# Performance work log

Measured on AMD Instinct MI355X. Metric: run time of the kernel, lower is better.

Reference implementation:

```python
import jax, jax.numpy as jnp
import numpy as np

HEADS = 4
KSIZE = 3
EPS = 1e-5


def conv2d(x, w, b, stride=1, padding=0, dilation=1):
    out = jax.lax.conv_general_dilated(
        x, w, (stride, stride), [(padding, padding)] * 2,
        rhs_dilation=(dilation, dilation),
        dimension_numbers=('NCHW', 'OIHW', 'NCHW'))
    return out + b[None, :, None, None]


def conv1x1(x, w, b):
    # w: (O, I, 1, 1)
    return jnp.einsum('oi,bihw->bohw', w[:, :, 0, 0], x) + b[None, :, None, None]


def batchnorm(x, gamma, beta, mean, var):
    inv = jax.lax.rsqrt(var + EPS)
    return (x - mean[None, :, None, None]) * (inv * gamma)[None, :, None, None] + beta[None, :, None, None]


def lrelu(x):
    return jax.nn.leaky_relu(x, 0.05)


def sasa(kv1, qmap, kv2, Wq, bq, Wkv, bkv):
    b, c, h, w = qmap.shape
    d = Wq.shape[0] // HEADS
    scale = d ** -0.5
    q = conv1x1(qmap, Wq, bq)                                   # b (n d) h w
    q = q.reshape(b, HEADS, d, h * w).transpose(0, 1, 3, 2) * scale  # b n x d

    def branch(kvmap):
        # pad BEFORE 1x1 conv (padded pixels attend with value = bias), matching torch
        p = jnp.pad(kvmap, ((0, 0), (0, 0), (1, 1), (1, 1)))
        kvp = conv1x1(p, Wkv, bkv)                              # b (n d) h+2 w+2
        # sliding 3x3 windows (k=v in the original: to_kv applied twice to same input)
        wins = jnp.stack([kvp[:, :, i:i + h, j:j + w]
                          for i in range(KSIZE) for j in range(KSIZE)], axis=2)  # b nd 9 h w
        kv = wins.reshape(b, HEADS, d, KSIZE * KSIZE, h * w).transpose(0, 1, 4, 3, 2)  # b n x y d
        logits = jnp.einsum('bnxd,bnxyd->bnxy', q, kv)
        wgt = jax.nn.softmax(logits, axis=-1)
        return jnp.einsum('bnxy,bnxyd->bnxd', wgt, kv)

    out = (branch(kv1) + branch(kv2)) * 0.5                     # b n x d
    return out.transpose(0, 1, 3, 2).reshape(b, HEADS * d, h, w)


def setup_inputs() -> dict:
    key = jax.random.key(0)
    ks = jax.random.split(key, 12)
    B, Cin, Cout, H, W = 2, 64, 128, 128, 128
    f32 = jnp.float32
    inp = {
        'x0': jax.random.normal(ks[0], (B, Cin, H, W), f32),
        'x1': jax.random.normal(ks[1], (B, Cin, H, W), f32),
        'x2': jax.random.normal(ks[2], (B, Cin, H, W), f32),
        # BN params (eval mode, reps=2)
        'gamma0': jnp.ones((Cin,), f32), 'beta0': jnp.zeros((Cin,), f32),
        'mean0': jnp.zeros((Cin,), f32), 'var0': jnp.ones((Cin,), f32),
        'gamma1': jnp.ones((Cout,), f32), 'beta1': jnp.zeros((Cout,), f32),
        'mean1': jnp.zeros((Cout,), f32), 'var1': jnp.ones((Cout,), f32),
        # channel-adjust 1x1 conv (residual path, i==0)
        'W_adj': jax.random.normal(ks[3], (Cout, Cin, 1, 1), f32) * 0.05,
        'b_adj': jnp.zeros((Cout,), f32),
        # 3x3 dilated convs
        'W_conv0': jax.random.normal(ks[4], (Cout, Cin, 3, 3), f32) * 0.05,
        'b_conv0': jnp.zeros((Cout,), f32),
        'W_conv1': jax.random.normal(ks[5], (Cout, Cout, 3, 3), f32) * 0.05,
        'b_conv1': jnp.zeros((Cout,), f32),
        # SASA projections
        'Wq': jax.random.normal(ks[6], (Cout, Cout, 1, 1), f32) * 0.05,
        'bq': jnp.zeros((Cout,), f32),
        'Wkv': jax.random.normal(ks[7], (Cout, Cout, 1, 1), f32) * 0.05,
        'bkv': jnp.zeros((Cout,), f32),
        # conv pooling (3x3 stride 2 pad 1)
        'W_pool': jax.random.normal(ks[8], (Cout, Cout, 3, 3), f32) * 0.05,
        'b_pool': jnp.zeros((Cout,), f32),
    }
    return inp


def reference(x0, x1, x2,
              gamma0, beta0, mean0, var0, gamma1, beta1, mean1, var1,
              W_adj, b_adj, W_conv0, b_conv0, W_conv1, b_conv1,
              Wq, bq, Wkv, bkv, W_pool, b_pool):
    dil = 1

    def rep(x, i):
        if i == 0:
            x = batchnorm(x, gamma0, beta0, mean0, var0)
            res = conv1x1(x, W_adj, b_adj)
            x = conv2d(x, W_conv0, b_conv0, 1, dil, dil)
        else:
            x = batchnorm(x, gamma1, beta1, mean1, var1)
            res = x
            x = conv2d(x, W_conv1, b_conv1, 1, dil, dil)
        return lrelu(x + res)

    n0, n1, n2 = x0, x1, x2
    for i in range(2):
        n0 = rep(n0, i)
        n1 = rep(n1, i)
        n2 = rep(n2, i)

    n1 = sasa(n0, n1, n2, Wq, bq, Wkv, bkv)
    pass_layer = n1
    n0 = conv2d(n0, W_pool, b_pool, stride=2, padding=1)
    n1 = conv2d(n1, W_pool, b_pool, stride=2, padding=1)
    n2 = conv2d(n2, W_pool, b_pool, stride=2, padding=1)
    return (n0, n1, n2, pass_layer)
```

## Files before the change

### kernel.cpp

```cpp
#include <hip/hip_runtime.h>
#include <cstdint>
#include <cstddef>

typedef __bf16 bf16x8 __attribute__((ext_vector_type(8)));
typedef float f32x4 __attribute__((ext_vector_type(4)));
typedef unsigned short u16x8 __attribute__((ext_vector_type(8)));
typedef unsigned int u32x4 __attribute__((ext_vector_type(4)));

#define AS1 __attribute__((address_space(1)))
#define AS3 __attribute__((address_space(3)))

__device__ __forceinline__ void gload16(const void* g, void* l) {
    __builtin_amdgcn_global_load_lds((AS1 unsigned int*)(unsigned long long)g,
                                     (AS3 unsigned int*)l, 16, 0, 0);
}

__device__ __forceinline__ unsigned short f2b(float f) {
    unsigned u = __builtin_bit_cast(unsigned, f);
    return (unsigned short)((u + 0x7fffu + ((u >> 16) & 1u)) >> 16);
}
__device__ __forceinline__ float b2f(unsigned short h) {
    return __builtin_bit_cast(float, ((unsigned)h) << 16);
}

static constexpr int HW = 16384;

__global__ __launch_bounds__(256) void zero_borders_kernel(
    unsigned short* X0, unsigned short* X1, unsigned short* X2,
    unsigned short* F0, unsigned short* F1, unsigned short* F2,
    unsigned short* G0, unsigned short* G1, unsigned short* G2)
{
    int z = blockIdx.z;
    unsigned short* p; int C;
    switch (z) {
        case 0: p = X0; C = 64; break;
        case 1: p = X1; C = 64; break;
        case 2: p = X2; C = 64; break;
        case 3: p = F0; C = 128; break;
        case 4: p = F1; C = 128; break;
        case 5: p = F2; C = 128; break;
        case 6: p = G0; C = 128; break;
        case 7: p = G1; C = 128; break;
        default: p = G2; C = 128; break;
    }
    int chunks = C >> 3;
    int total = 2 * 516 * chunks;
    int idx = blockIdx.x * 256 + threadIdx.x;
    if (idx >= total) return;
    int cb = idx % chunks;
    int pidx = idx / chunks;
    int n = pidx / 516;
    int b = pidx % 516;
    int y, x;
    if (b < 130)      { y = 0;       x = b; }
    else if (b < 260) { y = 129;     x = b - 130; }
    else if (b < 388) { y = b - 259; x = 0; }
    else              { y = b - 387; x = 129; }
    u32x4 zz = {0u, 0u, 0u, 0u};
    *(u32x4*)(p + ((size_t)((n * 130 + y) * 130 + x)) * C + cb * 8) = zz;
}

__global__ __launch_bounds__(256) void zero_one_kernel(unsigned short* p)
{
    int idx = blockIdx.x * 256 + threadIdx.x;
    if (idx >= 2 * 516 * 16) return;
    int cb = idx & 15;
    int pidx = idx >> 4;
    int n = pidx / 516;
    int b = pidx % 516;
    int y, x;
    if (b < 130)      { y = 0;       x = b; }
    else if (b < 260) { y = 129;     x = b - 130; }
    else if (b < 388) { y = b - 259; x = 0; }
    else              { y = b - 387; x = 129; }
    u32x4 zz = {0u, 0u, 0u, 0u};
    *(u32x4*)(p + ((size_t)((n * 130 + y) * 130 + x)) * 128 + cb * 8) = zz;
}

__global__ __launch_bounds__(256) void pack_kernel(
    const float* Wc0, const float* Wadj, const float* Wc1,
    const float* Wq, const float* Wkv, const float* Wpool,
    const float* bc0, const float* badj,
    const float* g1, const float* be1, const float* m1, const float* v1,
    unsigned short* W0p, unsigned short* W1p, unsigned short* Wqp,
    unsigned short* Wkvp, unsigned short* Wpp,
    float* b0sum, float* s1a, float* t1a)
{
    int z = blockIdx.z;
    int idx = blockIdx.x * 256 + threadIdx.x;
    if (z == 5) {
        if (idx < 128) {
            int co = idx;
            b0sum[co] = bc0[co] + badj[co];
            float s = g1[co] * rsqrtf(v1[co] + 1e-5f);
            s1a[co] = s;
            t1a[co] = be1[co] - m1[co] * s;
        }
        return;
    }
    int CIN, NTAP; unsigned short* dst;
    switch (z) {
        case 0: CIN = 64;  NTAP = 10; dst = W0p;  break;
        case 1: CIN = 128; NTAP = 10; dst = W1p;  break;
        case 2: CIN = 128; NTAP = 1;  dst = Wqp;  break;
        case 3: CIN = 128; NTAP = 1;  dst = Wkvp; break;
        default: CIN = 128; NTAP = 9; dst = Wpp;  break;
    }
    int KCN = CIN / 32;
    int count = NTAP * KCN * 512;
    if (idx >= count) return;
    int lane = idx & 63;
    int m = (idx >> 6) & 7;
    int rest = idx >> 9;
    int kc = rest % KCN;
    int tap = rest / KCN;
    int co = m * 16 + (lane & 15);
    int cib = kc * 32 + ((lane >> 4) << 3);
    unsigned short vals[8];
#pragma unroll
    for (int j = 0; j < 8; ++j) {
        int ci = cib + j;
        float v;
        if (z == 0)       v = (tap < 9) ? Wc0[((size_t)co * 64 + ci) * 9 + tap] : Wadj[co * 64 + ci];
        else if (z == 1)  v = (tap < 9) ? Wc1[((size_t)co * 128 + ci) * 9 + tap] : (co == ci ? 1.0f : 0.0f);
        else if (z == 2)  v = Wq[co * 128 + ci];
        else if (z == 3)  v = Wkv[co * 128 + ci];
        else              v = Wpool[((size_t)co * 128 + ci) * 9 + tap];
        vals[j] = f2b(v);
    }
    u32x4 pk;
    pk.x = vals[0] | ((unsigned)vals[1] << 16);
    pk.y = vals[2] | ((unsigned)vals[3] << 16);
    pk.z = vals[4] | ((unsigned)vals[5] << 16);
    pk.w = vals[6] | ((unsigned)vals[7] << 16);
    *(u32x4*)(dst + (size_t)idx * 8) = pk;
}

__global__ __launch_bounds__(256) void prep_kernel(
    const float* x0, const float* x1, const float* x2,
    const float* g0, const float* be0, const float* me0, const float* va0,
    unsigned short* X0, unsigned short* X1, unsigned short* X2)
{
    const int y = blockIdx.x;
    const int mz = blockIdx.y;
    const int map = mz >> 1, n = mz & 1;
    const float* in = (map == 0 ? x0 : map == 1 ? x1 : x2) + (size_t)n * 64 * HW + y * 128;
    unsigned short* out = (map == 0 ? X0 : map == 1 ? X1 : X2)
                          + ((size_t)(n * 130 + y + 1) * 130 + 1) * 64;
    const int x = threadIdx.x & 127;
    for (int cb = threadIdx.x >> 7; cb < 8; cb += 2) {
        unsigned short vals[8];
#pragma unroll
        for (int j = 0; j < 8; ++j) {
            int ci = cb * 8 + j;
            float s = g0[ci] * rsqrtf(va0[ci] + 1e-5f);
            float t = be0[ci] - me0[ci] * s;
            vals[j] = f2b(in[(size_t)ci * HW + x] * s + t);
        }
        u32x4 pk;
        pk.x = vals[0] | ((unsigned)vals[1] << 16);
        pk.y = vals[2] | ((unsigned)vals[3] << 16);
        pk.z = vals[4] | ((unsigned)vals[5] << 16);
        pk.w = vals[6] | ((unsigned)vals[7] << 16);
        *(u32x4*)(out + (size_t)x * 64 + cb * 8) = pk;
    }
}

template <int CIN, int EPI>
__global__ __launch_bounds__(256, 6) void conv3_kernel(
    const unsigned short* I0, const unsigned short* I1, const unsigned short* I2,
    const unsigned short* Wp, const float* bA, const float* bB, const float* bC,
    unsigned short* O0, unsigned short* O1, unsigned short* O2)
{
    constexpr int KCN = CIN / 32;
    constexpr int TKY[10] = {0,0,0,1,1,1,2,2,2,1};
    constexpr int TKX[10] = {0,1,2,0,1,2,0,1,2,1};
    const int tid = threadIdx.x;
    const int lane = tid & 63;
    const int l15 = lane & 15, l4 = lane >> 4;
    const int wv = tid >> 6;
    const int pxh = wv & 1;
    const int coq = wv >> 1;
    const int bid = blockIdx.x;
    const int wid = (bid & 7) * 192 + (bid >> 3);
    const int ch = wid & 1;
    const int y  = (wid >> 1) & 127;
    const int mz = wid >> 8;
    const int map = mz >> 1, n = mz & 1;
    const unsigned short* In = (map == 0 ? I0 : map == 1 ? I1 : I2) + (size_t)n * 130 * 130 * CIN;
    unsigned short* On = (map == 0 ? O0 : map == 1 ? O1 : O2) + (size_t)n * 130 * 130 * 128;

    __shared__ __align__(16) unsigned short stage[3 * 130 * 4 * 8];

    f32x4 acc[2][4];
#pragma unroll
    for (int a = 0; a < 2; ++a)
#pragma unroll
        for (int b = 0; b < 4; ++b) acc[a][b] = (f32x4){0.f, 0.f, 0.f, 0.f};

    const int px0 = pxh * 64;
    const u32x4* Ap = (const u32x4*)Wp;

    for (int kc = 0; kc < KCN; ++kc) {
        if (kc) __syncthreads();
        for (int idx = tid; idx < 1560; idx += 256) {
            int r = idx / 520;
            int rem = idx - r * 520;
            int xx = rem >> 2;
            int slot = rem & 3;
            int cd = slot ^ ((xx >> 1) & 3);
            const unsigned short* src = In + ((size_t)(y + r) * 130 + xx) * CIN + kc * 32 + cd * 8;
            gload16(src, stage + (size_t)(idx & ~63) * 8);
        }
        __syncthreads();
#pragma unroll
        for (int t = 0; t < 10; ++t) {
            const int ky = TKY[t], kx = TKX[t];
            u32x4 a[2];
#pragma unroll
            for (int mi = 0; mi < 2; ++mi)
                a[mi] = Ap[((size_t)(t * KCN + kc) * 8 + ch * 4 + coq * 2 + mi) * 64 + lane];
            bf16x8 bv[4];
#pragma unroll
            for (int nf = 0; nf < 4; ++nf) {
                int xx = px0 + nf * 16 + l15 + kx;
                int slot = l4 ^ ((xx >> 1) & 3);
                bv[nf] = *(const bf16x8*)(stage + ((size_t)(ky * 130 + xx) * 4 + slot) * 8);
            }
#pragma unroll
            for (int mi = 0; mi < 2; ++mi) {
                bf16x8 av = __builtin_bit_cast(bf16x8, a[mi]);
#pragma unroll
                for (int nf = 0; nf < 4; ++nf)
                    acc[mi][nf] = __builtin_amdgcn_mfma_f32_16x16x32_bf16(av, bv[nf], acc[mi][nf], 0, 0, 0);
            }
        }
    }
#pragma unroll
    for (int mi = 0; mi < 2; ++mi) {
#pragma unroll
        for (int nf = 0; nf < 4; ++nf) {
            int px = px0 + nf * 16 + l15;
            int cobase = (ch * 4 + coq * 2 + mi) * 16 + l4 * 4;
            float t4[4];
#pragma unroll
            for (int r = 0; r < 4; ++r) {
                int co = cobase + r;
                float v = acc[mi][nf][r] + bA[co];
                v = v > 0.f ? v : 0.05f * v;
                if (EPI == 0) v = v * bB[co] + bC[co];
                t4[r] = v;
            }
            unsigned short* op = On + ((size_t)(y + 1) * 130 + (px + 1)) * 128 + cobase;
            *(unsigned*)(op)     = (unsigned)f2b(t4[0]) | ((unsigned)f2b(t4[1]) << 16);
            *(unsigned*)(op + 2) = (unsigned)f2b(t4[2]) | ((unsigned)f2b(t4[3]) << 16);
        }
    }
}

__global__ __launch_bounds__(256, 4) void proj_kernel(
    const unsigned short* G0, const unsigned short* G1, const unsigned short* G2,
    const unsigned short* Wqp, const unsigned short* Wkvp,
    const float* bq, const float* bkv,
    unsigned short* KV0, unsigned short* KV2, unsigned short* Qb)
{
    const int z = blockIdx.z;
    const int proj = z >> 1, n = z & 1;
    const int yy = blockIdx.y;
    if (proj == 2 && (yy == 0 || yy == 129)) return;
    const int tid = threadIdx.x;
    const int lane = tid & 63, l15 = lane & 15, l4 = lane >> 4, wv = tid >> 6;
    const int ch = blockIdx.x;
    const unsigned short* In = (proj == 0 ? G0 : proj == 1 ? G2 : G1) + (size_t)n * 130 * 130 * 128;
    const unsigned short* Wp = (proj == 2) ? Wqp : Wkvp;
    const float* bias = (proj == 2) ? bq : bkv;

    __shared__ __align__(16) unsigned short stage[130 * 4 * 8];

    f32x4 acc[4][2];
#pragma unroll
    for (int a = 0; a < 4; ++a)
#pragma unroll
        for (int b = 0; b < 2; ++b) acc[a][b] = (f32x4){0.f, 0.f, 0.f, 0.f};

    const int px0 = wv * 32;
    const u32x4* Ap = (const u32x4*)Wp;

    for (int kc = 0; kc < 4; ++kc) {
        if (kc) __syncthreads();
        for (int idx = tid; idx < 520; idx += 256) {
            int xx = idx >> 2, slot = idx & 3;
            int cd = slot ^ ((xx >> 1) & 3);
            gload16(In + ((size_t)yy * 130 + xx) * 128 + kc * 32 + cd * 8,
                    stage + (size_t)(idx & ~63) * 8);
        }
        __syncthreads();
        u32x4 a[4];
#pragma unroll
        for (int mi = 0; mi < 4; ++mi)
            a[mi] = Ap[((size_t)kc * 8 + ch * 4 + mi) * 64 + lane];
        bf16x8 bv[2];
#pragma unroll
        for (int nf = 0; nf < 2; ++nf) {
            int xx = px0 + nf * 16 + l15 + 1;
            int slot = l4 ^ ((xx >> 1) & 3);
            bv[nf] = *(const bf16x8*)(stage + ((size_t)xx * 4 + slot) * 8);
        }
#pragma unroll
        for (int mi = 0; mi < 4; ++mi) {
            bf16x8 av = __builtin_bit_cast(bf16x8, a[mi]);
#pragma unroll
            for (int nf = 0; nf < 2; ++nf)
                acc[mi][nf] = __builtin_amdgcn_mfma_f32_16x16x32_bf16(av, bv[nf], acc[mi][nf], 0, 0, 0);
        }
        if (kc < 3) __syncthreads();
    }
#pragma unroll
    for (int mi = 0; mi < 4; ++mi) {
#pragma unroll
        for (int nf = 0; nf < 2; ++nf) {
            int px = px0 + nf * 16 + l15;
            int cobase = (ch * 4 + mi) * 16 + l4 * 4;
            float t4[4];
#pragma unroll
            for (int r = 0; r < 4; ++r) t4[r] = acc[mi][nf][r] + bias[cobase + r];
            unsigned short* op;
            if (proj == 2)
                op = Qb + ((size_t)(n * 128 + yy - 1) * 128 + px) * 128 + cobase;
            else
                op = (proj == 0 ? KV0 : KV2) + ((size_t)(n * 130 + yy) * 130 + (px + 1)) * 128 + cobase;
            *(unsigned*)(op)     = (unsigned)f2b(t4[0]) | ((unsigned)f2b(t4[1]) << 16);
            *(unsigned*)(op + 2) = (unsigned)f2b(t4[2]) | ((unsigned)f2b(t4[3]) << 16);
        }
    }
}

__global__ __launch_bounds__(256) void kv_border_kernel(
    unsigned short* KV0, unsigned short* KV2, const float* bkv)
{
    int idx = blockIdx.x * 256 + threadIdx.x;
    if (idx >= 16640) return;
    int cb = idx & 15;
    int t = idx >> 4;
    int col = t & 1; t >>= 1;
    int yy = t % 130; t /= 130;
    int n = t & 1;
    int buf = t >> 1;
    unsigned short* p = (buf ? KV2 : KV0)
        + ((size_t)(n * 130 + yy) * 130 + (col ? 129 : 0)) * 128 + cb * 8;
    u16x8 v;
#pragma unroll
    for (int j = 0; j < 8; ++j) v[j] = f2b(bkv[cb * 8 + j]);
    *(u16x8*)p = v;
}

__global__ __launch_bounds__(128) void attn_kernel(
    const unsigned short* Qb, const unsigned short* KV0,
    const unsigned short* KV2, unsigned short* P0, unsigned short* P1)
{
    const int bid = blockIdx.x;
    const int wid = (bid & 7) * 256 + (bid >> 3);
    const int br  = wid & 1;
    const int r2  = wid >> 1;
    const int n   = r2 >> 9;
    const int rem = r2 & 511;
    const int yt  = rem >> 3;
    const int xt  = rem & 7;
    const int y0  = yt * 2;
    const int x0  = xt * 16;

    const int tid = threadIdx.x;
    const int h   = tid & 3;
    const int pxl = (tid >> 2) & 15;
    const int py  = tid >> 6;
    const int x   = x0 + pxl;
    const int y   = y0 + py;
    const float SC = 0.17677669529663687f;

    const unsigned short* KV = br ? KV2 : KV0;
    unsigned short* Pb = br ? P1 : P0;

    __shared__ __align__(16) unsigned short kvb[4 * 20 * 128];

#pragma unroll
    for (int it = 0; it < 10; ++it) {
        int idx = it * 128 + tid;
        int g = idx >> 6, l = idx & 63;
        int r = g / 5, s = g - r * 5;
        int px = s * 4 + (l >> 4);
        int c  = (l & 15) ^ (px & 7);
        gload16(KV + (((size_t)(n * 130 + y0 + r) * 130) + x0 + px) * 128 + c * 8,
                kvb + (size_t)g * 512);
    }

    float qf[32];
    {
        const u16x8* qp = (const u16x8*)(Qb + (((size_t)(n * 128 + y) * 128 + x) * 128) + h * 32);
#pragma unroll
        for (int d8 = 0; d8 < 4; ++d8) {
            u16x8 q8 = qp[d8];
#pragma unroll
            for (int j = 0; j < 8; ++j) qf[d8 * 8 + j] = b2f(q8[j]) * SC;
        }
    }
    __syncthreads();

    float lg[9];
#pragma unroll
    for (int t = 0; t < 9; ++t) {
        int ky = t / 3, kx = t % 3;
        int pxw = pxl + kx;
        const unsigned short* base = kvb + ((size_t)(py + ky) * 20 + pxw) * 128;
        float s = 0.f;
#pragma unroll
        for (int d8 = 0; d8 < 4; ++d8) {
            int c = ((h << 2) | d8) ^ (pxw & 7);
            u16x8 kk = *(const u16x8*)(base + c * 8);
#pragma unroll
            for (int j = 0; j < 8; ++j) s += qf[d8 * 8 + j] * b2f(kk[j]);
        }
        lg[t] = s;
    }
    float mv = lg[0];
#pragma unroll
    for (int t = 1; t < 9; ++t) mv = fmaxf(mv, lg[t]);
    float w[9], sum = 0.f;
#pragma unroll
    for (int t = 0; t < 9; ++t) { w[t] = __expf(lg[t] - mv); sum += w[t]; }
    float r = 0.5f / sum;
#pragma unroll
    for (int t = 0; t < 9; ++t) w[t] *= r;

    float o[32];
#pragma unroll
    for (int d = 0; d < 32; ++d) o[d] = 0.f;
#pragma unroll
    for (int t = 0; t < 9; ++t) {
        int ky = t / 3, kx = t % 3;
        int pxw = pxl + kx;
        const unsigned short* base = kvb + ((size_t)(py + ky) * 20 + pxw) * 128;
#pragma unroll
        for (int d8 = 0; d8 < 4; ++d8) {
            int c = ((h << 2) | d8) ^ (pxw & 7);
            u16x8 kk = *(const u16x8*)(base + c * 8);
#pragma unroll
            for (int j = 0; j < 8; ++j) o[d8 * 8 + j] += w[t] * b2f(kk[j]);
        }
    }

    unsigned short* ap = Pb + ((size_t)(n * 130 + y + 1) * 130 + (x + 1)) * 128 + h * 32;
#pragma unroll
    for (int d8 = 0; d8 < 4; ++d8) {
        u16x8 v;
#pragma unroll
        for (int j = 0; j < 8; ++j) v[j] = f2b(o[d8 * 8 + j]);
        *(u16x8*)(ap + d8 * 8) = v;
    }
}

__global__ __launch_bounds__(256) void expand_kernel(
    const unsigned short* P0, const unsigned short* P1,
    unsigned short* A1p, float* pass)
{
    const int y = blockIdx.x, n = blockIdx.y;
    const int t = threadIdx.x;
    __shared__ float lds[128][129];

    const int px = t >> 1, ch0 = (t & 1) * 64;
    size_t off = ((size_t)(n * 130 + y + 1) * 130 + px + 1) * 128 + ch0;
    const u16x8* a = (const u16x8*)(P0 + off);
    const u16x8* b = (const u16x8*)(P1 + off);
    u16x8* o = (u16x8*)(A1p + off);
    float* lrow = &lds[px][ch0];
#pragma unroll
    for (int k = 0; k < 8; ++k) {
        u16x8 va = a[k], vb = b[k];
        u16x8 vo;
#pragma unroll
        for (int j = 0; j < 8; ++j) {
            float s = b2f(va[j]) + b2f(vb[j]);
            lrow[k * 8 + j] = s;
            vo[j] = f2b(s);
        }
        o[k] = vo;
    }
    __syncthreads();

    const int c = t >> 1, xh = t & 1;
    float* dst = pass + ((size_t)(n * 128 + c) * HW) + y * 128 + xh * 64;
#pragma unroll
    for (int i = 0; i < 16; ++i) {
        f32x4 q = { lds[xh * 64 + i * 4 + 0][c], lds[xh * 64 + i * 4 + 1][c],
                    lds[xh * 64 + i * 4 + 2][c], lds[xh * 64 + i * 4 + 3][c] };
        *(f32x4*)(dst + i * 4) = q;
    }
}

__global__ __launch_bounds__(256, 4) void pool_kernel(
    const unsigned short* G0, const unsigned short* A1, const unsigned short* G2,
    const unsigned short* Wpp, const float* bp, float* out)
{
    const int bid = blockIdx.x;
    const int wid = (bid & 7) * 96 + (bid >> 3);
    const int ch = wid & 1;
    const int yo = (wid >> 1) & 63;
    const int mz = wid >> 7;
    const int map = mz >> 1, n = mz & 1;
    const int tid = threadIdx.x, lane = tid & 63, l15 = lane & 15, l4 = lane >> 4, wv = tid >> 6;
    const int pxh = wv & 1, coq = wv >> 1;
    const unsigned short* In = (map == 0 ? G0 : map == 1 ? A1 : G2) + (size_t)n * 130 * 130 * 128;
    float* outp = out + (size_t)map * 1048576 + (size_t)n * 524288;

    __shared__ __align__(16) unsigned short stage[3 * 130 * 4 * 8];

    f32x4 acc[2][2];
#pragma unroll
    for (int a = 0; a < 2; ++a)
#pragma unroll
        for (int b = 0; b < 2; ++b) acc[a][b] = (f32x4){0.f, 0.f, 0.f, 0.f};

    const int px0 = pxh * 32;
    const u32x4* Ap = (const u32x4*)Wpp;

    for (int kc = 0; kc < 4; ++kc) {
        if (kc) __syncthreads();
        for (int idx = tid; idx < 1560; idx += 256) {
            int r = idx / 520;
            int rem = idx - r * 520;
            int xx = rem >> 2;
            int slot = rem & 3;
            int cd = slot ^ ((xx >> 1) & 3);
            gload16(In + ((size_t)(2 * yo + r) * 130 + xx) * 128 + kc * 32 + cd * 8,
                    stage + (size_t)(idx & ~63) * 8);
        }
        __syncthreads();
#pragma unroll
        for (int t = 0; t < 9; ++t) {
            const int ky = t / 3, kx = t % 3;
            u32x4 a[2];
#pragma unroll
            for (int mi = 0; mi < 2; ++mi)
                a[mi] = Ap[((size_t)(t * 4 + kc) * 8 + ch * 4 + coq * 2 + mi) * 64 + lane];
            bf16x8 bv[2];
#pragma unroll
            for (int nf = 0; nf < 2; ++nf) {
                int xx = 2 * (px0 + nf * 16 + l15) + kx;
                int slot = l4 ^ ((xx >> 1) & 3);
                bv[nf] = *(const bf16x8*)(stage + ((size_t)(ky * 130 + xx) * 4 + slot) * 8);
            }
#pragma unroll
            for (int mi = 0; mi < 2; ++mi) {
                bf16x8 av = __builtin_bit_cast(bf16x8, a[mi]);
#pragma unroll
                for (int nf = 0; nf < 2; ++nf)
                    acc[mi][nf] = __builtin_amdgcn_mfma_f32_16x16x32_bf16(av, bv[nf], acc[mi][nf], 0, 0, 0);
            }
        }
    }
#pragma unroll
    for (int mi = 0; mi < 2; ++mi) {
#pragma unroll
        for (int nf = 0; nf < 2; ++nf) {
            int cobase = (ch * 4 + coq * 2 + mi) * 16 + l4 * 4;
            int px = px0 + nf * 16 + l15;
#pragma unroll
            for (int r = 0; r < 4; ++r) {
                int co = cobase + r;
                outp[((size_t)co * 64 + yo) * 64 + px] = acc[mi][nf][r] + bp[co];
            }
        }
    }
}

extern "C" void kernel_launch(void* const* d_in, const int* in_sizes, int n_in,
                              void* d_out, int out_size, void* d_ws, size_t ws_size,
                              hipStream_t stream)
{
    const float* x0 = (const float*)d_in[0];
    const float* x1 = (const float*)d_in[1];
    const float* x2 = (const float*)d_in[2];
    const float* gamma0 = (const float*)d_in[3];
    const float* beta0  = (const float*)d_in[4];
    const float* mean0  = (const float*)d_in[5];
    const float* var0   = (const float*)d_in[6];
    const float* gamma1 = (const float*)d_in[7];
    const float* beta1  = (const float*)d_in[8];
    const float* mean1  = (const float*)d_in[9];
    const float* var1   = (const float*)d_in[10];
    const float* W_adj  = (const float*)d_in[11];
    const float* b_adj  = (const float*)d_in[12];
    const float* W_conv0 = (const float*)d_in[13];
    const float* b_conv0 = (const float*)d_in[14];
    const float* W_conv1 = (const float*)d_in[15];
    const float* b_conv1 = (const float*)d_in[16];
    const float* Wq  = (const float*)d_in[17];
    const float* bq  = (const float*)d_in[18];
    const float* Wkv = (const float*)d_in[19];
    const float* bkv = (const float*)d_in[20];
    const float* W_pool = (const float*)d_in[21];
    const float* b_pool = (const float*)d_in[22];

    float* out  = (float*)d_out;
    float* pass = out + 3145728;

    char* wsb = (char*)d_ws;
    const size_t FSZ = 8652800;
    const size_t XSZ = 4326400;
    unsigned short* F0 = (unsigned short*)(wsb);
    unsigned short* F1 = (unsigned short*)(wsb + FSZ);
    unsigned short* F2 = (unsigned short*)(wsb + 2 * FSZ);
    unsigned short* G0 = (unsigned short*)(wsb + 3 * FSZ);
    unsigned short* G1 = (unsigned short*)(wsb + 4 * FSZ);
    unsigned short* G2 = (unsigned short*)(wsb + 5 * FSZ);
    unsigned short* X0 = (unsigned short*)(wsb + 6 * FSZ);
    unsigned short* X1 = (unsigned short*)(wsb + 6 * FSZ + XSZ);
    unsigned short* X2 = (unsigned short*)(wsb + 6 * FSZ + 2 * XSZ);
    char* WAR = wsb + 6 * FSZ + 3 * XSZ;
    unsigned short* W0p    = (unsigned short*)(WAR);
    unsigned short* W1p    = (unsigned short*)(WAR + 163840);
    unsigned short* Wqp    = (unsigned short*)(WAR + 491520);
    unsigned short* Wkvp   = (unsigned short*)(WAR + 524288);
    unsigned short* Wpoolp = (unsigned short*)(WAR + 557056);
    float* b0sum = (float*)(WAR + 851968);
    float* s1a   = (float*)(WAR + 852480);
    float* t1a   = (float*)(WAR + 852992);
    unsigned short* KV0 = F0;
    unsigned short* KV2 = F1;
    unsigned short* Qb  = F2;
    unsigned short* P0  = G1;
    unsigned short* P1  = X0;
    unsigned short* A1p = F0;

    zero_borders_kernel<<<dim3(65, 1, 9), 256, 0, stream>>>(X0, X1, X2, F0, F1, F2, G0, G1, G2);
    pack_kernel<<<dim3(80, 1, 6), 256, 0, stream>>>(
        W_conv0, W_adj, W_conv1, Wq, Wkv, W_pool, b_conv0, b_adj,
        gamma1, beta1, mean1, var1, W0p, W1p, Wqp, Wkvp, Wpoolp, b0sum, s1a, t1a);
    prep_kernel<<<dim3(128, 6), 256, 0, stream>>>(
        x0, x1, x2, gamma0, beta0, mean0, var0, X0, X1, X2);

    conv3_kernel<64, 0><<<dim3(1536), 256, 0, stream>>>(
        X0, X1, X2, W0p, b0sum, s1a, t1a, F0, F1, F2);
    conv3_kernel<128, 1><<<dim3(1536), 256, 0, stream>>>(
        F0, F1, F2, W1p, b_conv1, nullptr, nullptr, G0, G1, G2);

    proj_kernel<<<dim3(2, 130, 6), 256, 0, stream>>>(
        G0, G1, G2, Wqp, Wkvp, bq, bkv, KV0, KV2, Qb);
    kv_border_kernel<<<dim3(65), 256, 0, stream>>>(KV0, KV2, bkv);

    attn_kernel<<<dim3(2048), 128, 0, stream>>>(Qb, KV0, KV2, P0, P1);

    zero_one_kernel<<<dim3(65), 256, 0, stream>>>(A1p);
    expand_kernel<<<dim3(128, 2), 256, 0, stream>>>(P0, P1, A1p, pass);

    pool_kernel<<<dim3(768), 256, 0, stream>>>(G0, A1p, G2, Wpoolp, b_pool, out);
}
```

Baseline: 172.0 us.

## Split conv3 rows into half-width tiles and double-buffer LDS staging

Each conv3 block now covers half a row (64 pixels) instead of a full row, so the grid doubles to 3072 blocks and each wave does half the MFMA work. Input staging moves into two LDS buffers, and the next channel chunk is prefetched with global_load_lds while the current one is computed, using vmcnt waits and raw s_barrier in place of __syncthreads. This targets global-load latency exposed between chunks and raises the number of blocks available to fill CUs. In exchange, the 2-pixel halo is loaded twice per row, per-block weight (A operand) loads double in total, and the vmcnt(3) count must match the per-thread load count exactly to stay correct.

```diff
diff --git a/kernel.cpp b/kernel.cpp
--- a/kernel.cpp
+++ b/kernel.cpp
@@ -182,37 +182,56 @@
     const int pxh = wv & 1;
     const int coq = wv >> 1;
     const int bid = blockIdx.x;
-    const int wid = (bid & 7) * 192 + (bid >> 3);
+    const int wid = (bid & 7) * 384 + (bid >> 3);
     const int ch = wid & 1;
-    const int y  = (wid >> 1) & 127;
-    const int mz = wid >> 8;
+    const int xh = (wid >> 1) & 1;
+    const int y  = (wid >> 2) & 127;
+    const int mz = wid >> 9;
     const int map = mz >> 1, n = mz & 1;
+    const int gx0 = xh * 64;
     const unsigned short* In = (map == 0 ? I0 : map == 1 ? I1 : I2) + (size_t)n * 130 * 130 * CIN;
     unsigned short* On = (map == 0 ? O0 : map == 1 ? O1 : O2) + (size_t)n * 130 * 130 * 128;
 
-    __shared__ __align__(16) unsigned short stage[3 * 130 * 4 * 8];
-
-    f32x4 acc[2][4];
+    __shared__ __align__(16) unsigned short stage[2 * 6528];
+
+    f32x4 acc[2][2];
 #pragma unroll
     for (int a = 0; a < 2; ++a)
 #pragma unroll
-        for (int b = 0; b < 4; ++b) acc[a][b] = (f32x4){0.f, 0.f, 0.f, 0.f};
-
-    const int px0 = pxh * 64;
+        for (int b = 0; b < 2; ++b) acc[a][b] = (f32x4){0.f, 0.f, 0.f, 0.f};
+
+    const int px0 = pxh * 32;
     const u32x4* Ap = (const u32x4*)Wp;
 
+    auto STAGE = [&](int buf, int kcc) {
+#pragma unroll
+        for (int it = 0; it < 4; ++it) {
+            int idx = it * 256 + tid;
+            if (idx < 816) {
+                int r = idx / 272;
+                int rem = idx - r * 272;
+                int xx = rem >> 2;
+                int slot = rem & 3;
+                int cd = slot ^ ((xx >> 1) & 3);
+                gload16(In + ((size_t)(y + r) * 130 + gx0 + xx) * CIN + kcc * 32 + cd * 8,
+                        stage + (size_t)buf * 6528 + (size_t)(idx & ~63) * 8);
+            }
+        }
+    };
+
+    STAGE(0, 0);
+
+#pragma unroll
     for (int kc = 0; kc < KCN; ++kc) {
-        if (kc) __syncthreads();
-        for (int idx = tid; idx < 1560; idx += 256) {
-            int r = idx / 520;
-            int rem = idx - r * 520;
-            int xx = rem >> 2;
-            int slot = rem & 3;
-            int cd = slot ^ ((xx >> 1) & 3);
-            const unsigned short* src = In + ((size_t)(y + r) * 130 + xx) * CIN + kc * 32 + cd * 8;
-            gload16(src, stage + (size_t)(idx & ~63) * 8);
-        }
-        __syncthreads();
+        if (kc + 1 < KCN) {
+            STAGE((kc + 1) & 1, kc + 1);
+            asm volatile("s_waitcnt vmcnt(3)" ::: "memory");
+        } else {
+            asm volatile("s_waitcnt vmcnt(0)" ::: "memory");
+        }
+        __builtin_amdgcn_s_barrier();
+        __builtin_amdgcn_sched_barrier(0);
+        const unsigned short* sb = stage + (size_t)(kc & 1) * 6528;
 #pragma unroll
         for (int t = 0; t < 10; ++t) {
             const int ky = TKY[t], kx = TKX[t];
@@ -220,27 +239,29 @@
 #pragma unroll
             for (int mi = 0; mi < 2; ++mi)
                 a[mi] = Ap[((size_t)(t * KCN + kc) * 8 + ch * 4 + coq * 2 + mi) * 64 + lane];
-            bf16x8 bv[4];
-#pragma unroll
-            for (int nf = 0; nf < 4; ++nf) {
+            bf16x8 bv[2];
+#pragma unroll
+            for (int nf = 0; nf < 2; ++nf) {
                 int xx = px0 + nf * 16 + l15 + kx;
                 int slot = l4 ^ ((xx >> 1) & 3);
-                bv[nf] = *(const bf16x8*)(stage + ((size_t)(ky * 130 + xx) * 4 + slot) * 8);
+                bv[nf] = *(const bf16x8*)(sb + ((size_t)(ky * 68 + xx) * 4 + slot) * 8);
             }
 #pragma unroll
             for (int mi = 0; mi < 2; ++mi) {
                 bf16x8 av = __builtin_bit_cast(bf16x8, a[mi]);
 #pragma unroll
-                for (int nf = 0; nf < 4; ++nf)
+                for (int nf = 0; nf < 2; ++nf)
                     acc[mi][nf] = __builtin_amdgcn_mfma_f32_16x16x32_bf16(av, bv[nf], acc[mi][nf], 0, 0, 0);
             }
         }
-    }
+        if (kc + 1 < KCN) __builtin_amdgcn_s_barrier();
+    }
+
 #pragma unroll
     for (int mi = 0; mi < 2; ++mi) {
 #pragma unroll
-        for (int nf = 0; nf < 4; ++nf) {
-            int px = px0 + nf * 16 + l15;
+        for (int nf = 0; nf < 2; ++nf) {
+            int px = gx0 + px0 + nf * 16 + l15;
             int cobase = (ch * 4 + coq * 2 + mi) * 16 + l4 * 4;
             float t4[4];
 #pragma unroll
@@ -638,9 +659,9 @@
     prep_kernel<<<dim3(128, 6), 256, 0, stream>>>(
         x0, x1, x2, gamma0, beta0, mean0, var0, X0, X1, X2);
 
-    conv3_kernel<64, 0><<<dim3(1536), 256, 0, stream>>>(
+    conv3_kernel<64, 0><<<dim3(3072), 256, 0, stream>>>(
         X0, X1, X2, W0p, b0sum, s1a, t1a, F0, F1, F2);
-    conv3_kernel<128, 1><<<dim3(1536), 256, 0, stream>>>(
+    conv3_kernel<128, 1><<<dim3(3072), 256, 0, stream>>>(
         F0, F1, F2, W1p, b_conv1, nullptr, nullptr, G0, G1, G2);
 
     proj_kernel<<<dim3(2, 130, 6), 256, 0, stream>>>(
```

Measured after the change: 181.3 us. 5.4% more time.
